# Performance work log

Measured on AMD Instinct MI355X. Metric: run time of the kernel, lower is better.

Reference implementation:

```python
import jax, jax.numpy as jnp
import numpy as np


def setup_inputs() -> dict:
    key = jax.random.key(0)
    k1, k2 = jax.random.split(key)
    B, N, M, D = 8, 8192, 8192, 3
    input1 = jax.random.normal(k1, (B, N, D), dtype=jnp.float32)
    input2 = jax.random.normal(k2, (B, M, D), dtype=jnp.float32)
    return {"input1": input1, "input2": input2}


def reference(input1, input2):
    # input1: [B, N, 3], input2: [B, M, 3]
    # Squared pairwise distances via ||x||^2 + ||y||^2 - 2<x,y>
    sq1 = jnp.sum(input1 * input1, axis=-1)          # [B, N]
    sq2 = jnp.sum(input2 * input2, axis=-1)          # [B, M]
    inner = jnp.einsum('bnd,bmd->bnm', input1, input2)  # [B, N, M]
    d = sq1[:, :, None] + sq2[:, None, :] - 2.0 * inner  # [B, N, M]
    d = jnp.maximum(d, 0.0)  # numerical guard
    dist1 = jnp.min(d, axis=2)  # [B, N] NN in input2 for each point of input1
    dist2 = jnp.min(d, axis=1)  # [B, M] NN in input1 for each point of input2
    loss = jnp.mean(dist1) + jnp.mean(dist2)
    return loss
```

## Files before the change

kernel.cpp:

```cpp
#include <hip/hip_runtime.h>


typedef _Float16 half8 __attribute__((ext_vector_type(8)));
typedef float    f16x  __attribute__((ext_vector_type(16)));

constexpr int B      = 8;
constexpr int NPTS   = 8192;
constexpr int TOTAL  = B * NPTS;
constexpr int NSTRIP = 256;
constexpr int NSTR   = NPTS / NSTRIP;
constexpr int MHALF  = 2048;
constexpr int NMH    = NPTS / MHALF;
constexpr int CHUNK  = 512;
constexpr int NCHUNK = MHALF / CHUNK;

__device__ __forceinline__ float colmin16(const f16x& a)
{
    float m0 = fminf(fminf(a[0],  a[1]),  a[2]);
    float m1 = fminf(fminf(a[3],  a[4]),  a[5]);
    float m2 = fminf(fminf(a[6],  a[7]),  a[8]);
    float m3 = fminf(fminf(a[9],  a[10]), a[11]);
    float m4 = fminf(fminf(a[12], a[13]), a[14]);
    return fminf(fminf(fminf(m0, m1), m2), fminf(fminf(m3, m4), a[15]));
}

__global__ __launch_bounds__(512) void chamfer_mfma(
    const float* __restrict__ in1, const float* __restrict__ in2,
    float* __restrict__ d1p, float* __restrict__ d2p, float* __restrict__ out)
{
    const int b     = blockIdx.z;
    const int strip = blockIdx.x;
    const int mh    = blockIdx.y;
    const int wave  = threadIdx.x >> 6;
    const int lane  = threadIdx.x & 63;
    const int col   = lane & 31;
    const int half  = lane >> 5;

    if ((blockIdx.x | blockIdx.y | blockIdx.z) == 0 && threadIdx.x == 0)
        *out = 0.0f;

    __shared__ _Float16 ldsLo[CHUNK * 8];
    __shared__ _Float16 ldsHi[CHUNK * 8];
    __shared__ unsigned d2lds[MHALF];

    for (int i = threadIdx.x; i < MHALF; i += 512)
        d2lds[i] = 0xFFFFFFFFu;

    const int nbase = strip * NSTRIP + wave * 32;
    half8 afrag;
    {
        const float* a = in1 + ((size_t)b * NPTS + nbase + col) * 3;
        float x = a[0], y = a[1], z = a[2];
        float sq = fmaf(x, x, fmaf(y, y, z * z));
        _Float16 xh = (_Float16)x, yh = (_Float16)y, zh = (_Float16)z;
        _Float16 xl = (_Float16)(x - (float)xh);
        _Float16 yl = (_Float16)(y - (float)yh);
        _Float16 zl = (_Float16)(z - (float)zh);
        _Float16 sh = (_Float16)sq, sl = (_Float16)(sq - (float)sh);
        half8 lo = {xh, yh, zh, xl, yl, zl, xh, yh};
        half8 hi = {zh, sh, sl, (_Float16)1.f, (_Float16)1.f,
                    (_Float16)0.f, (_Float16)0.f, (_Float16)0.f};
        afrag = half ? hi : lo;
    }

    f16x MN1, zero;
#pragma unroll
    for (int r = 0; r < 16; ++r) { MN1[r] = 1e30f; zero[r] = 0.0f; }

    const float* Craw = in2 + ((size_t)b * NPTS + mh * MHALF) * 3;

    for (int c = 0; c < NCHUNK; ++c) {
        __syncthreads();
        {
            const float* cp = Craw + (size_t)(c * CHUNK + threadIdx.x) * 3;
            float cx = cp[0], cy = cp[1], cz = cp[2];
            float x = -2.f * cx, y = -2.f * cy, z = -2.f * cz;
            float sq = fmaf(cx, cx, fmaf(cy, cy, cz * cz));
            _Float16 xh = (_Float16)x, yh = (_Float16)y, zh = (_Float16)z;
            _Float16 xl = (_Float16)(x - (float)xh);
            _Float16 yl = (_Float16)(y - (float)yh);
            _Float16 zl = (_Float16)(z - (float)zh);
            _Float16 sh = (_Float16)sq, sl = (_Float16)(sq - (float)sh);
            half8 lo = {xh, yh, zh, xh, yh, zh, xl, yl};
            half8 hi = {zl, (_Float16)1.f, (_Float16)1.f, sh, sl,
                        (_Float16)0.f, (_Float16)0.f, (_Float16)0.f};
            *(half8*)&ldsLo[threadIdx.x * 8] = lo;
            *(half8*)&ldsHi[threadIdx.x * 8] = hi;
        }
        __syncthreads();

        const _Float16* fragBase = half ? ldsHi : ldsLo;
#pragma unroll 2
        for (int t = 0; t < CHUNK / 32; t += 2) {
            half8 bfA = *(const half8*)&fragBase[((t    ) * 32 + col) * 8];
            half8 bfB = *(const half8*)&fragBase[((t + 1) * 32 + col) * 8];
            f16x accA = __builtin_amdgcn_mfma_f32_32x32x16_f16(afrag, bfA, zero, 0, 0, 0);
            f16x accB = __builtin_amdgcn_mfma_f32_32x32x16_f16(afrag, bfB, zero, 0, 0, 0);

#pragma unroll
            for (int r = 0; r < 16; ++r)
                MN1[r] = fminf(fminf(MN1[r], accA[r]), accB[r]);

            float vA = fmaxf(colmin16(accA), 0.0f);
            atomicMin(&d2lds[c * CHUNK + t * 32 + col], __float_as_uint(vA));
            float vB = fmaxf(colmin16(accB), 0.0f);
            atomicMin(&d2lds[c * CHUNK + (t + 1) * 32 + col], __float_as_uint(vB));
        }
    }
    __syncthreads();

    float* d2 = d2p + ((size_t)b * NSTR + strip) * NPTS + mh * MHALF;
    for (int i = threadIdx.x; i < MHALF; i += 512)
        d2[i] = __uint_as_float(d2lds[i]);

#pragma unroll
    for (int m = 1; m <= 16; m <<= 1)
#pragma unroll
        for (int r = 0; r < 16; ++r)
            MN1[r] = fminf(MN1[r], __shfl_xor(MN1[r], m, 64));
    if (col == 0) {
        float* d1 = d1p + ((size_t)b * NMH + mh) * NPTS;
#pragma unroll
        for (int r = 0; r < 16; ++r)
            d1[nbase + (r & 3) + 8 * (r >> 2) + 4 * half] = MN1[r];
    }
}

__global__ __launch_bounds__(256) void reduce_kernel(
    const float* __restrict__ d1p, const float* __restrict__ d2p,
    float* __restrict__ out)
{
    int g  = blockIdx.x * 256 + threadIdx.x;
    int b  = g >> 11;
    int mq = g & 2047;

    const float4* p2 = (const float4*)(d2p + (size_t)b * NSTR * NPTS) + mq;
    float4 v2 = p2[0];
#pragma unroll
    for (int s = 1; s < NSTR; ++s) {
        float4 t = p2[(size_t)s * (NPTS / 4)];
        v2.x = fminf(v2.x, t.x); v2.y = fminf(v2.y, t.y);
        v2.z = fminf(v2.z, t.z); v2.w = fminf(v2.w, t.w);
    }
    float4 a0 = ((const float4*)(d1p + ((size_t)b * NMH + 0) * NPTS))[mq];
    float4 a1 = ((const float4*)(d1p + ((size_t)b * NMH + 1) * NPTS))[mq];
    float4 a2 = ((const float4*)(d1p + ((size_t)b * NMH + 2) * NPTS))[mq];
    float4 a3 = ((const float4*)(d1p + ((size_t)b * NMH + 3) * NPTS))[mq];
    float v = fmaxf(fminf(fminf(a0.x, a1.x), fminf(a2.x, a3.x)), 0.0f)
            + fmaxf(fminf(fminf(a0.y, a1.y), fminf(a2.y, a3.y)), 0.0f)
            + fmaxf(fminf(fminf(a0.z, a1.z), fminf(a2.z, a3.z)), 0.0f)
            + fmaxf(fminf(fminf(a0.w, a1.w), fminf(a2.w, a3.w)), 0.0f)
            + v2.x + v2.y + v2.z + v2.w;

#pragma unroll
    for (int off = 32; off; off >>= 1)
        v += __shfl_down(v, off, 64);
    __shared__ float wsum[4];
    int lane = threadIdx.x & 63, w = threadIdx.x >> 6;
    if (lane == 0) wsum[w] = v;
    __syncthreads();
    if (threadIdx.x == 0)
        atomicAdd(out, (wsum[0] + wsum[1] + wsum[2] + wsum[3]) *
                           (1.0f / (float)TOTAL));
}

extern "C" void kernel_launch(void* const* d_in, const int* in_sizes, int n_in,
                              void* d_out, int out_size, void* d_ws, size_t ws_size,
                              hipStream_t stream)
{
    const float* in1 = (const float*)d_in[0];
    const float* in2 = (const float*)d_in[1];
    float* out = (float*)d_out;

    char* ws = (char*)d_ws;
    float* d1p = (float*)ws;
    float* d2p = (float*)(ws + (size_t)NMH * TOTAL * 4);

    chamfer_mfma<<<dim3(NPTS / NSTRIP, NMH, B), 512, 0, stream>>>(
        in1, in2, d1p, d2p, out);
    reduce_kernel<<<TOTAL / 1024, 256, 0, stream>>>(d1p, d2p, out);
}
```

Baseline: 94.09 us.

## Process two A row-tiles per wave to reuse B fragments and halve atomics

Blocks shrink from 8 to 4 waves, and each wave now owns two 32-row A tiles (rows offset by 128), so the strip still covers 256 rows. Every B fragment read from LDS feeds two MFMAs, and the column minima of both tiles are merged before the LDS atomicMin, which halves the LDS reads and atomics per MFMA. In exchange each wave holds more accumulator registers, there are fewer waves per block to hide latency, and each thread packs twice as many staging points per chunk.

```diff
diff --git a/kernel.cpp b/kernel.cpp
--- a/kernel.cpp
+++ b/kernel.cpp
@@ -24,7 +24,22 @@
     return fminf(fminf(fminf(m0, m1), m2), fminf(fminf(m3, m4), a[15]));
 }
 
-__global__ __launch_bounds__(512) void chamfer_mfma(
+__device__ __forceinline__ half8 pack_a(const float* __restrict__ a, int half)
+{
+    float x = a[0], y = a[1], z = a[2];
+    float sq = fmaf(x, x, fmaf(y, y, z * z));
+    _Float16 xh = (_Float16)x, yh = (_Float16)y, zh = (_Float16)z;
+    _Float16 xl = (_Float16)(x - (float)xh);
+    _Float16 yl = (_Float16)(y - (float)yh);
+    _Float16 zl = (_Float16)(z - (float)zh);
+    _Float16 sh = (_Float16)sq, sl = (_Float16)(sq - (float)sh);
+    half8 lo = {xh, yh, zh, xl, yl, zl, xh, yh};
+    half8 hi = {zh, sh, sl, (_Float16)1.f, (_Float16)1.f,
+                (_Float16)0.f, (_Float16)0.f, (_Float16)0.f};
+    return half ? hi : lo;
+}
+
+__global__ __launch_bounds__(256) void chamfer_mfma(
     const float* __restrict__ in1, const float* __restrict__ in2,
     float* __restrict__ d1p, float* __restrict__ d2p, float* __restrict__ out)
 {
@@ -43,36 +58,26 @@
     __shared__ _Float16 ldsHi[CHUNK * 8];
     __shared__ unsigned d2lds[MHALF];
 
-    for (int i = threadIdx.x; i < MHALF; i += 512)
+    for (int i = threadIdx.x; i < MHALF; i += 256)
         d2lds[i] = 0xFFFFFFFFu;
 
-    const int nbase = strip * NSTRIP + wave * 32;
-    half8 afrag;
-    {
-        const float* a = in1 + ((size_t)b * NPTS + nbase + col) * 3;
-        float x = a[0], y = a[1], z = a[2];
-        float sq = fmaf(x, x, fmaf(y, y, z * z));
-        _Float16 xh = (_Float16)x, yh = (_Float16)y, zh = (_Float16)z;
-        _Float16 xl = (_Float16)(x - (float)xh);
-        _Float16 yl = (_Float16)(y - (float)yh);
-        _Float16 zl = (_Float16)(z - (float)zh);
-        _Float16 sh = (_Float16)sq, sl = (_Float16)(sq - (float)sh);
-        half8 lo = {xh, yh, zh, xl, yl, zl, xh, yh};
-        half8 hi = {zh, sh, sl, (_Float16)1.f, (_Float16)1.f,
-                    (_Float16)0.f, (_Float16)0.f, (_Float16)0.f};
-        afrag = half ? hi : lo;
-    }
-
-    f16x MN1, zero;
-#pragma unroll
-    for (int r = 0; r < 16; ++r) { MN1[r] = 1e30f; zero[r] = 0.0f; }
+    const int nbase0 = strip * NSTRIP + wave * 32;
+    const int nbase1 = nbase0 + 128;
+    half8 afrag0 = pack_a(in1 + ((size_t)b * NPTS + nbase0 + col) * 3, half);
+    half8 afrag1 = pack_a(in1 + ((size_t)b * NPTS + nbase1 + col) * 3, half);
+
+    f16x MN0, MN1, zero;
+#pragma unroll
+    for (int r = 0; r < 16; ++r) { MN0[r] = 1e30f; MN1[r] = 1e30f; zero[r] = 0.0f; }
 
     const float* Craw = in2 + ((size_t)b * NPTS + mh * MHALF) * 3;
 
     for (int c = 0; c < NCHUNK; ++c) {
         __syncthreads();
-        {
-            const float* cp = Craw + (size_t)(c * CHUNK + threadIdx.x) * 3;
+#pragma unroll
+        for (int s = 0; s < 2; ++s) {
+            const int k = threadIdx.x + s * 256;
+            const float* cp = Craw + (size_t)(c * CHUNK + k) * 3;
             float cx = cp[0], cy = cp[1], cz = cp[2];
             float x = -2.f * cx, y = -2.f * cy, z = -2.f * cz;
             float sq = fmaf(cx, cx, fmaf(cy, cy, cz * cz));
@@ -84,45 +89,58 @@
             half8 lo = {xh, yh, zh, xh, yh, zh, xl, yl};
             half8 hi = {zl, (_Float16)1.f, (_Float16)1.f, sh, sl,
                         (_Float16)0.f, (_Float16)0.f, (_Float16)0.f};
-            *(half8*)&ldsLo[threadIdx.x * 8] = lo;
-            *(half8*)&ldsHi[threadIdx.x * 8] = hi;
+            *(half8*)&ldsLo[k * 8] = lo;
+            *(half8*)&ldsHi[k * 8] = hi;
         }
         __syncthreads();
 
         const _Float16* fragBase = half ? ldsHi : ldsLo;
-#pragma unroll 2
+#pragma unroll 1
         for (int t = 0; t < CHUNK / 32; t += 2) {
             half8 bfA = *(const half8*)&fragBase[((t    ) * 32 + col) * 8];
             half8 bfB = *(const half8*)&fragBase[((t + 1) * 32 + col) * 8];
-            f16x accA = __builtin_amdgcn_mfma_f32_32x32x16_f16(afrag, bfA, zero, 0, 0, 0);
-            f16x accB = __builtin_amdgcn_mfma_f32_32x32x16_f16(afrag, bfB, zero, 0, 0, 0);
-
+
+            f16x accA0 = __builtin_amdgcn_mfma_f32_32x32x16_f16(afrag0, bfA, zero, 0, 0, 0);
+            f16x accB0 = __builtin_amdgcn_mfma_f32_32x32x16_f16(afrag0, bfB, zero, 0, 0, 0);
 #pragma unroll
             for (int r = 0; r < 16; ++r)
-                MN1[r] = fminf(fminf(MN1[r], accA[r]), accB[r]);
-
-            float vA = fmaxf(colmin16(accA), 0.0f);
+                MN0[r] = fminf(fminf(MN0[r], accA0[r]), accB0[r]);
+            float vA = colmin16(accA0);
+            float vB = colmin16(accB0);
+
+            f16x accA1 = __builtin_amdgcn_mfma_f32_32x32x16_f16(afrag1, bfA, zero, 0, 0, 0);
+            f16x accB1 = __builtin_amdgcn_mfma_f32_32x32x16_f16(afrag1, bfB, zero, 0, 0, 0);
+#pragma unroll
+            for (int r = 0; r < 16; ++r)
+                MN1[r] = fminf(fminf(MN1[r], accA1[r]), accB1[r]);
+            vA = fmaxf(fminf(vA, colmin16(accA1)), 0.0f);
+            vB = fmaxf(fminf(vB, colmin16(accB1)), 0.0f);
+
             atomicMin(&d2lds[c * CHUNK + t * 32 + col], __float_as_uint(vA));
-            float vB = fmaxf(colmin16(accB), 0.0f);
             atomicMin(&d2lds[c * CHUNK + (t + 1) * 32 + col], __float_as_uint(vB));
         }
     }
     __syncthreads();
 
     float* d2 = d2p + ((size_t)b * NSTR + strip) * NPTS + mh * MHALF;
-    for (int i = threadIdx.x; i < MHALF; i += 512)
+    for (int i = threadIdx.x; i < MHALF; i += 256)
         d2[i] = __uint_as_float(d2lds[i]);
 
 #pragma unroll
     for (int m = 1; m <= 16; m <<= 1)
 #pragma unroll
-        for (int r = 0; r < 16; ++r)
+        for (int r = 0; r < 16; ++r) {
+            MN0[r] = fminf(MN0[r], __shfl_xor(MN0[r], m, 64));
             MN1[r] = fminf(MN1[r], __shfl_xor(MN1[r], m, 64));
+        }
     if (col == 0) {
         float* d1 = d1p + ((size_t)b * NMH + mh) * NPTS;
 #pragma unroll
-        for (int r = 0; r < 16; ++r)
-            d1[nbase + (r & 3) + 8 * (r >> 2) + 4 * half] = MN1[r];
+        for (int r = 0; r < 16; ++r) {
+            int row = (r & 3) + 8 * (r >> 2) + 4 * half;
+            d1[nbase0 + row] = MN0[r];
+            d1[nbase1 + row] = MN1[r];
+        }
     }
 }
 
@@ -176,7 +194,7 @@
     float* d1p = (float*)ws;
     float* d2p = (float*)(ws + (size_t)NMH * TOTAL * 4);
 
-    chamfer_mfma<<<dim3(NPTS / NSTRIP, NMH, B), 512, 0, stream>>>(
+    chamfer_mfma<<<dim3(NPTS / NSTRIP, NMH, B), 256, 0, stream>>>(
         in1, in2, d1p, d2p, out);
     reduce_kernel<<<TOTAL / 1024, 256, 0, stream>>>(d1p, d2p, out);
 }
```

Measured after the change: 102.4 us. +8.8%, slower.
